# Performance work log

Measured on AMD Instinct MI355X. Metric: run time of the kernel, lower is better.

## Reference

```python
import jax, jax.numpy as jnp
import numpy as np


def _log_g(x):
    # log of g(x) = where(x>=0, x+0.5, sigmoid(x)), computed stably in log space
    return jnp.where(x >= 0.0, jnp.log(jax.nn.relu(x) + 0.5), -jax.nn.softplus(-x))


def setup_inputs() -> dict:
    key = jax.random.key(0)
    k1, k2, k3, k4 = jax.random.split(key, 4)
    B, T, D, H = 4, 8192, 512, 512
    x = jax.random.normal(k1, (B, T, D), dtype=jnp.float32)
    h_prev = jax.random.uniform(k2, (B, 1, H), dtype=jnp.float32)  # positive: log(h0) taken
    W_h = jax.random.normal(k3, (H, D), dtype=jnp.float32) * (1.0 / np.sqrt(D))
    b_h = jnp.zeros((H,), dtype=jnp.float32)
    W_z = jax.random.normal(k4, (H, D), dtype=jnp.float32) * (1.0 / np.sqrt(D))
    b_z = jnp.zeros((H,), dtype=jnp.float32)
    return {"x": x, "h_prev": h_prev, "W_h": W_h, "b_h": b_h, "W_z": W_z, "b_z": b_z}


def reference(x, h_prev, W_h, b_h, W_z, b_z):
    # parallel (seq_len > 1) minGRU forward via Heinsen log-space scan
    k = jnp.einsum('btd,hd->bth', x, W_z) + b_z           # (B,T,H) gate pre-activation
    log_z = -jax.nn.softplus(-k)                          # log sigmoid(k)
    log_coeffs = -jax.nn.softplus(k)                      # log (1 - sigmoid(k))
    log_tilde_h = _log_g(jnp.einsum('btd,hd->bth', x, W_h) + b_h)
    log_h0 = jnp.log(h_prev)                              # (B,1,H)
    log_values = jnp.concatenate([log_h0, log_z + log_tilde_h], axis=1)  # (B,T+1,H)
    # a_star = [0, cumsum(log_coeffs)]
    a_star = jnp.pad(jnp.cumsum(log_coeffs, axis=1), ((0, 0), (1, 0), (0, 0)))
    log_h = a_star + jax.lax.cumlogsumexp(log_values - a_star, axis=1)
    h = jnp.exp(log_h)[:, 1:]                             # drop h0 -> (B,T,H)
    return h
```

## Files before the change

kernel.cpp:

```cpp
#include <hip/hip_runtime.h>
#include <hip/hip_bf16.h>
#include <stdint.h>

#define B_ 4
#define T_ 8192
#define D_ 512
#define H_ 512
#define M_ (B_ * T_)
#define SEG 32
#define SPB 256
#define NSEG (M_ / SEG)

typedef __attribute__((ext_vector_type(8))) short short8;
typedef __attribute__((ext_vector_type(4))) float floatx4;
typedef __attribute__((ext_vector_type(2))) float float2e;

__device__ __forceinline__ unsigned short f2bf(float f) {
    union { float f; unsigned int u; } v; v.f = f;
    unsigned int u = v.u;
    u += 0x7fffu + ((u >> 16) & 1u);
    return (unsigned short)(u >> 16);
}
__device__ __forceinline__ float bf_lo(unsigned int u) {
    union { unsigned int i; float f; } a; a.i = u << 16; return a.f;
}
__device__ __forceinline__ float bf_hi(unsigned int u) {
    union { unsigned int i; float f; } a; a.i = u & 0xffff0000u; return a.f;
}
__device__ __forceinline__ unsigned int pk_cd(float c, float d) {
    return (unsigned int)f2bf(c) | ((unsigned int)f2bf(d) << 16);
}

#define X8 (M_ * D_ / 8)
#define W8 (H_ * D_ / 8)

__global__ __launch_bounds__(256)
void conv_all(const float* __restrict__ x,
              const float* __restrict__ Wz,
              const float* __restrict__ Wh,
              unsigned short* __restrict__ xbf,
              unsigned short* __restrict__ Wf)
{
    const int gid    = blockIdx.x * blockDim.x + threadIdx.x;
    const int stride = gridDim.x * blockDim.x;
    for (int i = gid; i < X8; i += stride) {
        floatx4 a = __builtin_nontemporal_load((const floatx4*)x + 2 * i);
        floatx4 b = __builtin_nontemporal_load((const floatx4*)x + 2 * i + 1);
        short8 w;
        w[0] = (short)f2bf(a[0]); w[1] = (short)f2bf(a[1]);
        w[2] = (short)f2bf(a[2]); w[3] = (short)f2bf(a[3]);
        w[4] = (short)f2bf(b[0]); w[5] = (short)f2bf(b[1]);
        w[6] = (short)f2bf(b[2]); w[7] = (short)f2bf(b[3]);
        *((short8*)xbf + i) = w;
    }
    if (gid < 2 * W8) {
        const int i = gid;
        const float* src = (i < W8) ? Wz : Wh;
        const int idx = (i < W8) ? i : i - W8;
        floatx4 a = __builtin_nontemporal_load((const floatx4*)src + 2 * idx);
        floatx4 b = __builtin_nontemporal_load((const floatx4*)src + 2 * idx + 1);
        short8 w;
        w[0] = (short)f2bf(a[0]); w[1] = (short)f2bf(a[1]);
        w[2] = (short)f2bf(a[2]); w[3] = (short)f2bf(a[3]);
        w[4] = (short)f2bf(b[0]); w[5] = (short)f2bf(b[1]);
        w[6] = (short)f2bf(b[2]); w[7] = (short)f2bf(b[3]);
        *((short8*)Wf + i) = w;
    }
}

#define LDSB 32768

__global__ __launch_bounds__(256, 4)
void gemm_cd(const unsigned short* __restrict__ xbf,
             const unsigned short* __restrict__ Wf,
             const float* __restrict__ bz, const float* __restrict__ bh,
             unsigned int* __restrict__ cd,
             float2* __restrict__ Sagg)
{
    __shared__ __align__(16) char smem[LDSB];
    unsigned short* lds = (unsigned short*)smem;
    unsigned int*   cdl = (unsigned int*)smem;

    const int tid  = threadIdx.x;
    const int lane = tid & 63;
    const int wave = tid >> 6;
    const int xcd  = blockIdx.x & 7;
    const int nblk = (blockIdx.x >> 3) & 7;
    const int mblk = xcd * 32 + (blockIdx.x >> 6);
    const int m0 = mblk * 128;
    const int n0 = nblk * 64;
    const int wm = (wave >> 1) * 64;
    const int wn = (wave & 1) * 32;
    const int l15  = lane & 15;
    const int quad = lane >> 4;
    const int srow = lane >> 2;
    const int sp   = lane & 3;

    #define STAGE(p, kt)                                                          \
    {                                                                             \
        const int kb = (kt) * 32;                                                 \
        unsigned short* bb = lds + (p) * 8192;                                    \
        _Pragma("unroll")                                                         \
        for (int r = 0; r < 2; ++r) {                                             \
            const int chunk = r * 4 + wave;                                       \
            const int row   = chunk * 16 + srow;                                  \
            const int kp    = sp ^ (row & 3);                                     \
            __builtin_amdgcn_global_load_lds(                                     \
                (const __attribute__((address_space(1))) unsigned int*)           \
                    (xbf + (size_t)(m0 + row) * D_ + kb + kp * 8),                \
                (__attribute__((address_space(3))) unsigned int*)(bb + chunk * 512),\
                16, 0, 0);                                                        \
        }                                                                         \
        {                                                                         \
            const int row = wave * 16 + srow;                                     \
            const int kp  = sp ^ (row & 3);                                       \
            __builtin_amdgcn_global_load_lds(                                     \
                (const __attribute__((address_space(1))) unsigned int*)           \
                    (Wf + (size_t)(n0 + row) * D_ + kb + kp * 8),                 \
                (__attribute__((address_space(3))) unsigned int*)(bb + 4096 + wave * 512),\
                16, 0, 0);                                                        \
            __builtin_amdgcn_global_load_lds(                                     \
                (const __attribute__((address_space(1))) unsigned int*)           \
                    (Wf + (size_t)(512 + n0 + row) * D_ + kb + kp * 8),           \
                (__attribute__((address_space(3))) unsigned int*)(bb + 6144 + wave * 512),\
                16, 0, 0);                                                        \
        }                                                                         \
    }

    floatx4 acc_z[4][2], acc_h[4][2];
    #pragma unroll
    for (int i = 0; i < 4; ++i)
        #pragma unroll
        for (int j = 0; j < 2; ++j) { acc_z[i][j] = (floatx4)0.0f; acc_h[i][j] = (floatx4)0.0f; }

    STAGE(0, 0);

    for (int kt = 0; kt < 16; ++kt) {
        __syncthreads();
        const int base = (kt & 1) * 8192;
        short8 af[4], zf[2], hf[2];
        #pragma unroll
        for (int i = 0; i < 4; ++i) {
            const int ra = wm + i * 16 + l15;
            af[i] = *(const short8*)&lds[base + ra * 32 + ((quad ^ (ra & 3)) * 8)];
        }
        #pragma unroll
        for (int j = 0; j < 2; ++j) {
            const int rb = wn + j * 16 + l15;
            zf[j] = *(const short8*)&lds[base + 4096 + rb * 32 + ((quad ^ (rb & 3)) * 8)];
            hf[j] = *(const short8*)&lds[base + 6144 + rb * 32 + ((quad ^ (rb & 3)) * 8)];
        }
        if (kt < 15) STAGE((kt + 1) & 1, kt + 1);
        #pragma unroll
        for (int i = 0; i < 4; ++i)
            #pragma unroll
            for (int j = 0; j < 2; ++j) {
                acc_z[i][j] = __builtin_amdgcn_mfma_f32_16x16x32_bf16(zf[j], af[i], acc_z[i][j], 0, 0, 0);
                acc_h[i][j] = __builtin_amdgcn_mfma_f32_16x16x32_bf16(hf[j], af[i], acc_h[i][j], 0, 0, 0);
            }
    }

    __syncthreads();

    #pragma unroll
    for (int j = 0; j < 2; ++j) {
        const int hlb = wn + j * 16 + quad * 4;
        const float4 bzv = *(const float4*)&bz[n0 + hlb];
        const float4 bhv = *(const float4*)&bh[n0 + hlb];
        #pragma unroll
        for (int i = 0; i < 4; ++i) {
            const int mloc = wm + i * 16 + l15;
            uint4 w;
            #pragma unroll
            for (int r = 0; r < 4; ++r) {
                float kz = acc_z[i][j][r] + ((const float*)&bzv)[r];
                float hp = acc_h[i][j][r] + ((const float*)&bhv)[r];
                float c  = 1.0f / (1.0f + __expf(kz));
                float g  = (hp >= 0.0f) ? (hp + 0.5f) : (1.0f / (1.0f + __expf(-hp)));
                float d  = (1.0f - c) * g;
                ((unsigned int*)&w)[r] = pk_cd(c, d);
            }
            *(uint4*)&cd[(size_t)(m0 + mloc) * H_ + n0 + hlb] = w;
            *(uint4*)&cdl[mloc * 64 + (hlb ^ ((mloc & 7) << 2))] = w;
        }
    }

    __syncthreads();

    {
        float C = 1.0f, Dv = 0.0f;
        const int t0 = wave * 32;
        #pragma unroll
        for (int t = 0; t < 32; ++t) {
            const int row = t0 + t;
            unsigned int u = cdl[row * 64 + (lane ^ ((row & 7) << 2))];
            float c = bf_lo(u), d = bf_hi(u);
            Dv = fmaf(c, Dv, d);
            C *= c;
        }
        const int chain = (m0 >> 13) * 512 + n0 + lane;
        const int seg   = ((m0 >> 5) & 255) + wave;
        Sagg[(size_t)chain * SPB + seg] = make_float2(C, Dv);
    }
    #undef STAGE
}

__global__ __launch_bounds__(256)
void interseg(const float* __restrict__ h_prev,
              const float2* __restrict__ Sagg,
              float* __restrict__ Hseg)
{
    const int chain = blockIdx.x * 4 + (threadIdx.x >> 6);
    const int lane  = threadIdx.x & 63;
    const float2* spp = Sagg + (size_t)chain * SPB + lane * 4;
    float4 q0 = *(const float4*)&spp[0];
    float4 q1 = *(const float4*)&spp[2];
    float C = q0.x, D = q0.y;
    D = fmaf(q0.z, D, q0.w);  C *= q0.z;
    D = fmaf(q1.x, D, q1.y);  C *= q1.x;
    D = fmaf(q1.z, D, q1.w);  C *= q1.z;
    #pragma unroll
    for (int off = 1; off < 64; off <<= 1) {
        float Cp = __shfl_up(C, off, 64);
        float Dp = __shfl_up(D, off, 64);
        if (lane >= off) { D = fmaf(C, Dp, D); C *= Cp; }
    }
    float Ce = __shfl_up(C, 1, 64);
    float De = __shfl_up(D, 1, 64);
    if (lane == 0) { Ce = 1.0f; De = 0.0f; }
    const float h0 = h_prev[chain];
    float hs = fmaf(Ce, h0, De);
    float4 o;
    o.x = hs;
    hs = fmaf(q0.x, hs, q0.y); o.y = hs;
    hs = fmaf(q0.z, hs, q0.w); o.z = hs;
    hs = fmaf(q1.x, hs, q1.y); o.w = hs;
    *(float4*)&Hseg[(size_t)chain * SPB + lane * 4] = o;
}

__global__ __launch_bounds__(256)
void apply_scan(const unsigned int* __restrict__ cd,
                const float* __restrict__ Hseg,
                float* __restrict__ out)
{
    const int sg = blockIdx.x;
    const int b  = sg >> 8;
    const int s  = sg & 255;
    const int h  = threadIdx.x * 2;
    const unsigned int* base = cd + (size_t)sg * SEG * H_ + h;
    float* ob = out + (size_t)sg * SEG * H_ + h;
    uint2 v[SEG];
    #pragma unroll
    for (int t = 0; t < SEG; ++t)
        v[t] = *(const uint2*)(base + (size_t)t * H_);
    float hs0 = Hseg[(size_t)(b * 512 + h)     * SPB + s];
    float hs1 = Hseg[(size_t)(b * 512 + h + 1) * SPB + s];
    #pragma unroll
    for (int t = 0; t < SEG; ++t) {
        hs0 = fmaf(bf_lo(v[t].x), hs0, bf_hi(v[t].x));
        hs1 = fmaf(bf_lo(v[t].y), hs1, bf_hi(v[t].y));
        float2e o; o.x = hs0; o.y = hs1;
        __builtin_nontemporal_store(o, (float2e*)(ob + (size_t)t * H_));
    }
}

extern "C" void kernel_launch(void* const* d_in, const int* in_sizes, int n_in,
                              void* d_out, int out_size, void* d_ws, size_t ws_size,
                              hipStream_t stream)
{
    const float* x      = (const float*)d_in[0];
    const float* h_prev = (const float*)d_in[1];
    const float* W_h    = (const float*)d_in[2];
    const float* b_h    = (const float*)d_in[3];
    const float* W_z    = (const float*)d_in[4];
    const float* b_z    = (const float*)d_in[5];
    float* out = (float*)d_out;

    unsigned short* xbf = (unsigned short*)d_out;

    char* ws = (char*)d_ws;
    unsigned int* cd = (unsigned int*)ws;
    size_t cd_bytes = (size_t)M_ * H_ * 4;
    unsigned short* Wf = (unsigned short*)(ws + cd_bytes);
    size_t wf_bytes = (size_t)2 * H_ * D_ * sizeof(unsigned short);
    float2* Sagg = (float2*)(ws + cd_bytes + wf_bytes);
    float*  Hseg = (float*)((char*)Sagg + (size_t)2048 * SPB * sizeof(float2));

    conv_all<<<dim3(2048), dim3(256), 0, stream>>>(x, W_z, W_h, xbf, Wf);
    gemm_cd<<<dim3((M_ / 128) * (H_ / 64)), dim3(256), 0, stream>>>(
        xbf, Wf, b_z, b_h, cd, Sagg);
    interseg<<<dim3(512), dim3(256), 0, stream>>>(h_prev, Sagg, Hseg);
    apply_scan<<<dim3(NSEG), dim3(256), 0, stream>>>(cd, Hseg, out);
}
```

Baseline: 197.9 us.

## Fuse GEMM, inter-segment scan and apply scan into one cooperative persistent kernel

```diff
diff --git a/kernel.cpp b/kernel.cpp
--- a/kernel.cpp
+++ b/kernel.cpp
@@ -1,6 +1,9 @@
 #include <hip/hip_runtime.h>
+#include <hip/hip_cooperative_groups.h>
 #include <hip/hip_bf16.h>
 #include <stdint.h>
+
+namespace cg = cooperative_groups;
 
 #define B_ 4
 #define T_ 8192
@@ -10,6 +13,7 @@
 #define SEG 32
 #define SPB 256
 #define NSEG (M_ / SEG)
+#define NTILE 2048
 
 typedef __attribute__((ext_vector_type(8))) short short8;
 typedef __attribute__((ext_vector_type(4))) float floatx4;
@@ -71,12 +75,16 @@
 #define LDSB 32768
 
 __global__ __launch_bounds__(256, 4)
-void gemm_cd(const unsigned short* __restrict__ xbf,
-             const unsigned short* __restrict__ Wf,
-             const float* __restrict__ bz, const float* __restrict__ bh,
-             unsigned int* __restrict__ cd,
-             float2* __restrict__ Sagg)
+void fused_gsa(const unsigned short* __restrict__ xbf,
+               const unsigned short* __restrict__ Wf,
+               const float* __restrict__ bz, const float* __restrict__ bh,
+               const float* __restrict__ h_prev,
+               unsigned int* __restrict__ cd,
+               float2* __restrict__ Sagg,
+               float* __restrict__ Hseg,
+               float* __restrict__ out)
 {
+    cg::grid_group grid = cg::this_grid();
     __shared__ __align__(16) char smem[LDSB];
     unsigned short* lds = (unsigned short*)smem;
     unsigned int*   cdl = (unsigned int*)smem;
@@ -84,183 +92,181 @@
     const int tid  = threadIdx.x;
     const int lane = tid & 63;
     const int wave = tid >> 6;
-    const int xcd  = blockIdx.x & 7;
-    const int nblk = (blockIdx.x >> 3) & 7;
-    const int mblk = xcd * 32 + (blockIdx.x >> 6);
-    const int m0 = mblk * 128;
-    const int n0 = nblk * 64;
-    const int wm = (wave >> 1) * 64;
-    const int wn = (wave & 1) * 32;
     const int l15  = lane & 15;
     const int quad = lane >> 4;
     const int srow = lane >> 2;
     const int sp   = lane & 3;
-
-    #define STAGE(p, kt)                                                          \
-    {                                                                             \
-        const int kb = (kt) * 32;                                                 \
-        unsigned short* bb = lds + (p) * 8192;                                    \
-        _Pragma("unroll")                                                         \
-        for (int r = 0; r < 2; ++r) {                                             \
-            const int chunk = r * 4 + wave;                                       \
-            const int row   = chunk * 16 + srow;                                  \
-            const int kp    = sp ^ (row & 3);                                     \
-            __builtin_amdgcn_global_load_lds(                                     \
-                (const __attribute__((address_space(1))) unsigned int*)           \
-                    (xbf + (size_t)(m0 + row) * D_ + kb + kp * 8),                \
-                (__attribute__((address_space(3))) unsigned int*)(bb + chunk * 512),\
-                16, 0, 0);                                                        \
-        }                                                                         \
-        {                                                                         \
-            const int row = wave * 16 + srow;                                     \
-            const int kp  = sp ^ (row & 3);                                       \
-            __builtin_amdgcn_global_load_lds(                                     \
-                (const __attribute__((address_space(1))) unsigned int*)           \
-                    (Wf + (size_t)(n0 + row) * D_ + kb + kp * 8),                 \
-                (__attribute__((address_space(3))) unsigned int*)(bb + 4096 + wave * 512),\
-                16, 0, 0);                                                        \
-            __builtin_amdgcn_global_load_lds(                                     \
-                (const __attribute__((address_space(1))) unsigned int*)           \
-                    (Wf + (size_t)(512 + n0 + row) * D_ + kb + kp * 8),           \
-                (__attribute__((address_space(3))) unsigned int*)(bb + 6144 + wave * 512),\
-                16, 0, 0);                                                        \
-        }                                                                         \
-    }
-
-    floatx4 acc_z[4][2], acc_h[4][2];
-    #pragma unroll
-    for (int i = 0; i < 4; ++i)
+    const int wm = (wave >> 1) * 64;
+    const int wn = (wave & 1) * 32;
+
+    #pragma unroll 1
+    for (int blk = blockIdx.x; blk < NTILE; blk += gridDim.x) {
+        const int xcd  = blk & 7;
+        const int nblk = (blk >> 3) & 7;
+        const int mblk = xcd * 32 + (blk >> 6);
+        const int m0 = mblk * 128;
+        const int n0 = nblk * 64;
+
+        #define STAGE(p, kt)                                                          \
+        {                                                                             \
+            const int kb = (kt) * 32;                                                 \
+            unsigned short* bb = lds + (p) * 8192;                                    \
+            _Pragma("unroll")                                                         \
+            for (int r = 0; r < 2; ++r) {                                             \
+                const int chunk = r * 4 + wave;                                       \
+                const int row   = chunk * 16 + srow;                                  \
+                const int kp    = sp ^ (row & 3);                                     \
+                __builtin_amdgcn_global_load_lds(                                     \
+                    (const __attribute__((address_space(1))) unsigned int*)           \
+                        (xbf + (size_t)(m0 + row) * D_ + kb + kp * 8),                \
+                    (__attribute__((address_space(3))) unsigned int*)(bb + chunk * 512),\
+                    16, 0, 0);                                                        \
+            }                                                                         \
+            {                                                                         \
+                const int row = wave * 16 + srow;                                     \
+                const int kp  = sp ^ (row & 3);                                       \
+                __builtin_amdgcn_global_load_lds(                                     \
+                    (const __attribute__((address_space(1))) unsigned int*)           \
+                        (Wf + (size_t)(n0 + row) * D_ + kb + kp * 8),                 \
+                    (__attribute__((address_space(3))) unsigned int*)(bb + 4096 + wave * 512),\
+                    16, 0, 0);                                                        \
+                __builtin_amdgcn_global_load_lds(                                     \
+                    (const __attribute__((address_space(1))) unsigned int*)           \
+                        (Wf + (size_t)(512 + n0 + row) * D_ + kb + kp * 8),           \
+                    (__attribute__((address_space(3))) unsigned int*)(bb + 6144 + wave * 512),\
+                    16, 0, 0);                                                        \
+            }                                                                         \
+        }
+
+        floatx4 acc_z[4][2], acc_h[4][2];
         #pragma unroll
-        for (int j = 0; j < 2; ++j) { acc_z[i][j] = (floatx4)0.0f; acc_h[i][j] = (floatx4)0.0f; }
-
-    STAGE(0, 0);
-
-    for (int kt = 0; kt < 16; ++kt) {
+        for (int i = 0; i < 4; ++i)
+            #pragma unroll
+            for (int j = 0; j < 2; ++j) { acc_z[i][j] = (floatx4)0.0f; acc_h[i][j] = (floatx4)0.0f; }
+
+        STAGE(0, 0);
+
+        for (int kt = 0; kt < 16; ++kt) {
+            __syncthreads();
+            const int base = (kt & 1) * 8192;
+            short8 af[4], zf[2], hf[2];
+            #pragma unroll
+            for (int i = 0; i < 4; ++i) {
+                const int ra = wm + i * 16 + l15;
+                af[i] = *(const short8*)&lds[base + ra * 32 + ((quad ^ (ra & 3)) * 8)];
+            }
+            #pragma unroll
+            for (int j = 0; j < 2; ++j) {
+                const int rb = wn + j * 16 + l15;
+                zf[j] = *(const short8*)&lds[base + 4096 + rb * 32 + ((quad ^ (rb & 3)) * 8)];
+                hf[j] = *(const short8*)&lds[base + 6144 + rb * 32 + ((quad ^ (rb & 3)) * 8)];
+            }
+            if (kt < 15) STAGE((kt + 1) & 1, kt + 1);
+            #pragma unroll
+            for (int i = 0; i < 4; ++i)
+                #pragma unroll
+                for (int j = 0; j < 2; ++j) {
+                    acc_z[i][j] = __builtin_amdgcn_mfma_f32_16x16x32_bf16(zf[j], af[i], acc_z[i][j], 0, 0, 0);
+                    acc_h[i][j] = __builtin_amdgcn_mfma_f32_16x16x32_bf16(hf[j], af[i], acc_h[i][j], 0, 0, 0);
+                }
+        }
+
         __syncthreads();
-        const int base = (kt & 1) * 8192;
-        short8 af[4], zf[2], hf[2];
-        #pragma unroll
-        for (int i = 0; i < 4; ++i) {
-            const int ra = wm + i * 16 + l15;
-            af[i] = *(const short8*)&lds[base + ra * 32 + ((quad ^ (ra & 3)) * 8)];
-        }
+
         #pragma unroll
         for (int j = 0; j < 2; ++j) {
-            const int rb = wn + j * 16 + l15;
-            zf[j] = *(const short8*)&lds[base + 4096 + rb * 32 + ((quad ^ (rb & 3)) * 8)];
-            hf[j] = *(const short8*)&lds[base + 6144 + rb * 32 + ((quad ^ (rb & 3)) * 8)];
-        }
-        if (kt < 15) STAGE((kt + 1) & 1, kt + 1);
+            const int hlb = wn + j * 16 + quad * 4;
+            const float4 bzv = *(const float4*)&bz[n0 + hlb];
+            const float4 bhv = *(const float4*)&bh[n0 + hlb];
+            #pragma unroll
+            for (int i = 0; i < 4; ++i) {
+                const int mloc = wm + i * 16 + l15;
+                uint4 w;
+                #pragma unroll
+                for (int r = 0; r < 4; ++r) {
+                    float kz = acc_z[i][j][r] + ((const float*)&bzv)[r];
+                    float hp = acc_h[i][j][r] + ((const float*)&bhv)[r];
+                    float c  = 1.0f / (1.0f + __expf(kz));
+                    float g  = (hp >= 0.0f) ? (hp + 0.5f) : (1.0f / (1.0f + __expf(-hp)));
+                    float d  = (1.0f - c) * g;
+                    ((unsigned int*)&w)[r] = pk_cd(c, d);
+                }
+                *(uint4*)&cd[(size_t)(m0 + mloc) * H_ + n0 + hlb] = w;
+                *(uint4*)&cdl[mloc * 64 + (hlb ^ ((mloc & 7) << 2))] = w;
+            }
+        }
+
+        __syncthreads();
+
+        {
+            float C = 1.0f, Dv = 0.0f;
+            const int t0 = wave * 32;
+            #pragma unroll
+            for (int t = 0; t < 32; ++t) {
+                const int row = t0 + t;
+                unsigned int u = cdl[row * 64 + (lane ^ ((row & 7) << 2))];
+                float c = bf_lo(u), d = bf_hi(u);
+                Dv = fmaf(c, Dv, d);
+                C *= c;
+            }
+            const int chain = (m0 >> 13) * 512 + n0 + lane;
+            const int seg   = ((m0 >> 5) & 255) + wave;
+            Sagg[(size_t)chain * SPB + seg] = make_float2(C, Dv);
+        }
+        __syncthreads();
+        #undef STAGE
+    }
+
+    grid.sync();
+
+    #pragma unroll 1
+    for (int cb = blockIdx.x; cb < 512; cb += gridDim.x) {
+        const int chain = cb * 4 + wave;
+        const float2* spp = Sagg + (size_t)chain * SPB + lane * 4;
+        float4 q0 = *(const float4*)&spp[0];
+        float4 q1 = *(const float4*)&spp[2];
+        float C = q0.x, D = q0.y;
+        D = fmaf(q0.z, D, q0.w);  C *= q0.z;
+        D = fmaf(q1.x, D, q1.y);  C *= q1.x;
+        D = fmaf(q1.z, D, q1.w);  C *= q1.z;
         #pragma unroll
-        for (int i = 0; i < 4; ++i)
-            #pragma unroll
-            for (int j = 0; j < 2; ++j) {
-                acc_z[i][j] = __builtin_amdgcn_mfma_f32_16x16x32_bf16(zf[j], af[i], acc_z[i][j], 0, 0, 0);
-                acc_h[i][j] = __builtin_amdgcn_mfma_f32_16x16x32_bf16(hf[j], af[i], acc_h[i][j], 0, 0, 0);
-            }
-    }
-
-    __syncthreads();
-
-    #pragma unroll
-    for (int j = 0; j < 2; ++j) {
-        const int hlb = wn + j * 16 + quad * 4;
-        const float4 bzv = *(const float4*)&bz[n0 + hlb];
-        const float4 bhv = *(const float4*)&bh[n0 + hlb];
+        for (int off = 1; off < 64; off <<= 1) {
+            float Cp = __shfl_up(C, off, 64);
+            float Dp = __shfl_up(D, off, 64);
+            if (lane >= off) { D = fmaf(C, Dp, D); C *= Cp; }
+        }
+        float Ce = __shfl_up(C, 1, 64);
+        float De = __shfl_up(D, 1, 64);
+        if (lane == 0) { Ce = 1.0f; De = 0.0f; }
+        const float h0 = h_prev[chain];
+        float hs = fmaf(Ce, h0, De);
+        float4 o;
+        o.x = hs;
+        hs = fmaf(q0.x, hs, q0.y); o.y = hs;
+        hs = fmaf(q0.z, hs, q0.w); o.z = hs;
+        hs = fmaf(q1.x, hs, q1.y); o.w = hs;
+        *(float4*)&Hseg[(size_t)chain * SPB + lane * 4] = o;
+    }
+
+    grid.sync();
+
+    #pragma unroll 1
+    for (int sg = blockIdx.x; sg < NSEG; sg += gridDim.x) {
+        const int b  = sg >> 8;
+        const int s  = sg & 255;
+        const int h  = tid * 2;
+        float hs0 = Hseg[(size_t)(b * 512 + h)     * SPB + s];
+        float hs1 = Hseg[(size_t)(b * 512 + h + 1) * SPB + s];
+        const unsigned int* base = cd + (size_t)sg * SEG * H_ + h;
+        float* ob = out + (size_t)sg * SEG * H_ + h;
         #pragma unroll
-        for (int i = 0; i < 4; ++i) {
-            const int mloc = wm + i * 16 + l15;
-            uint4 w;
-            #pragma unroll
-            for (int r = 0; r < 4; ++r) {
-                float kz = acc_z[i][j][r] + ((const float*)&bzv)[r];
-                float hp = acc_h[i][j][r] + ((const float*)&bhv)[r];
-                float c  = 1.0f / (1.0f + __expf(kz));
-                float g  = (hp >= 0.0f) ? (hp + 0.5f) : (1.0f / (1.0f + __expf(-hp)));
-                float d  = (1.0f - c) * g;
-                ((unsigned int*)&w)[r] = pk_cd(c, d);
-            }
-            *(uint4*)&cd[(size_t)(m0 + mloc) * H_ + n0 + hlb] = w;
-            *(uint4*)&cdl[mloc * 64 + (hlb ^ ((mloc & 7) << 2))] = w;
-        }
-    }
-
-    __syncthreads();
-
-    {
-        float C = 1.0f, Dv = 0.0f;
-        const int t0 = wave * 32;
-        #pragma unroll
-        for (int t = 0; t < 32; ++t) {
-            const int row = t0 + t;
-            unsigned int u = cdl[row * 64 + (lane ^ ((row & 7) << 2))];
-            float c = bf_lo(u), d = bf_hi(u);
-            Dv = fmaf(c, Dv, d);
-            C *= c;
-        }
-        const int chain = (m0 >> 13) * 512 + n0 + lane;
-        const int seg   = ((m0 >> 5) & 255) + wave;
-        Sagg[(size_t)chain * SPB + seg] = make_float2(C, Dv);
-    }
-    #undef STAGE
-}
-
-__global__ __launch_bounds__(256)
-void interseg(const float* __restrict__ h_prev,
-              const float2* __restrict__ Sagg,
-              float* __restrict__ Hseg)
-{
-    const int chain = blockIdx.x * 4 + (threadIdx.x >> 6);
-    const int lane  = threadIdx.x & 63;
-    const float2* spp = Sagg + (size_t)chain * SPB + lane * 4;
-    float4 q0 = *(const float4*)&spp[0];
-    float4 q1 = *(const float4*)&spp[2];
-    float C = q0.x, D = q0.y;
-    D = fmaf(q0.z, D, q0.w);  C *= q0.z;
-    D = fmaf(q1.x, D, q1.y);  C *= q1.x;
-    D = fmaf(q1.z, D, q1.w);  C *= q1.z;
-    #pragma unroll
-    for (int off = 1; off < 64; off <<= 1) {
-        float Cp = __shfl_up(C, off, 64);
-        float Dp = __shfl_up(D, off, 64);
-        if (lane >= off) { D = fmaf(C, Dp, D); C *= Cp; }
-    }
-    float Ce = __shfl_up(C, 1, 64);
-    float De = __shfl_up(D, 1, 64);
-    if (lane == 0) { Ce = 1.0f; De = 0.0f; }
-    const float h0 = h_prev[chain];
-    float hs = fmaf(Ce, h0, De);
-    float4 o;
-    o.x = hs;
-    hs = fmaf(q0.x, hs, q0.y); o.y = hs;
-    hs = fmaf(q0.z, hs, q0.w); o.z = hs;
-    hs = fmaf(q1.x, hs, q1.y); o.w = hs;
-    *(float4*)&Hseg[(size_t)chain * SPB + lane * 4] = o;
-}
-
-__global__ __launch_bounds__(256)
-void apply_scan(const unsigned int* __restrict__ cd,
-                const float* __restrict__ Hseg,
-                float* __restrict__ out)
-{
-    const int sg = blockIdx.x;
-    const int b  = sg >> 8;
-    const int s  = sg & 255;
-    const int h  = threadIdx.x * 2;
-    const unsigned int* base = cd + (size_t)sg * SEG * H_ + h;
-    float* ob = out + (size_t)sg * SEG * H_ + h;
-    uint2 v[SEG];
-    #pragma unroll
-    for (int t = 0; t < SEG; ++t)
-        v[t] = *(const uint2*)(base + (size_t)t * H_);
-    float hs0 = Hseg[(size_t)(b * 512 + h)     * SPB + s];
-    float hs1 = Hseg[(size_t)(b * 512 + h + 1) * SPB + s];
-    #pragma unroll
-    for (int t = 0; t < SEG; ++t) {
-        hs0 = fmaf(bf_lo(v[t].x), hs0, bf_hi(v[t].x));
-        hs1 = fmaf(bf_lo(v[t].y), hs1, bf_hi(v[t].y));
-        float2e o; o.x = hs0; o.y = hs1;
-        __builtin_nontemporal_store(o, (float2e*)(ob + (size_t)t * H_));
+        for (int t = 0; t < SEG; ++t) {
+            uint2 v = *(const uint2*)(base + (size_t)t * H_);
+            hs0 = fmaf(bf_lo(v.x), hs0, bf_hi(v.x));
+            hs1 = fmaf(bf_lo(v.y), hs1, bf_hi(v.y));
+            float2e o; o.x = hs0; o.y = hs1;
+            __builtin_nontemporal_store(o, (float2e*)(ob + (size_t)t * H_));
+        }
     }
 }
 
@@ -287,8 +293,27 @@
     float*  Hseg = (float*)((char*)Sagg + (size_t)2048 * SPB * sizeof(float2));
 
     conv_all<<<dim3(2048), dim3(256), 0, stream>>>(x, W_z, W_h, xbf, Wf);
-    gemm_cd<<<dim3((M_ / 128) * (H_ / 64)), dim3(256), 0, stream>>>(
-        xbf, Wf, b_z, b_h, cd, Sagg);
-    interseg<<<dim3(512), dim3(256), 0, stream>>>(h_prev, Sagg, Hseg);
-    apply_scan<<<dim3(NSEG), dim3(256), 0, stream>>>(cd, Hseg, out);
-}
+
+    int bpc = 0;
+    (void)hipOccupancyMaxActiveBlocksPerMultiprocessor(&bpc, (const void*)fused_gsa,
+                                                       256, 0);
+    if (bpc < 1) bpc = 1;
+    int grid = bpc * 256;
+    if (grid > 1024) grid = 1024;
+    if (grid < 256)  grid = 256;
+
+    const unsigned short* xbf_c = xbf;
+    const unsigned short* Wf_c  = Wf;
+    const float* bz_c = b_z;
+    const float* bh_c = b_h;
+    const float* hp_c = h_prev;
+    unsigned int* cd_c = cd;
+    float2* Sagg_c = Sagg;
+    float* Hseg_c = Hseg;
+    float* out_c = out;
+    void* args[] = { (void*)&xbf_c, (void*)&Wf_c, (void*)&bz_c, (void*)&bh_c,
+                     (void*)&hp_c, (void*)&cd_c, (void*)&Sagg_c, (void*)&Hseg_c,
+                     (void*)&out_c };
+    hipLaunchCooperativeKernel((void*)fused_gsa, dim3(grid), dim3(256),
+                               args, 0, stream);
+}
```

New measurement: 371.6 us. +87.7%, slower.
